# Kernel tuning notes

Measured on AMD Instinct MI355X. Metric: run time of the kernel, lower is better.

## Reference

```python
import jax, jax.numpy as jnp
import numpy as np
import math

B = 16384; IN_DIM = 512; OUT_DIM = 256
D_MODEL = 512; N_HEADS = 8; E_LAYERS = 3; D_FF = 2048
FACTOR = 5; EPS = 1e-5
E_HEAD = D_MODEL // N_HEADS


def setup_inputs() -> dict:
    key = jax.random.key(0)
    ks = jax.random.split(key, 16)
    def w(k, shape):
        return jax.random.normal(k, shape, dtype=jnp.float32) * 0.02
    return {
        "x": jax.random.normal(ks[0], (B, IN_DIM), dtype=jnp.float32),
        "w_in": w(ks[1], (IN_DIM, D_MODEL)), "b_in": jnp.zeros((D_MODEL,), jnp.float32),
        "wq": w(ks[2], (D_MODEL, D_MODEL)), "bq": jnp.zeros((D_MODEL,), jnp.float32),
        "wk": w(ks[3], (D_MODEL, D_MODEL)), "bk": jnp.zeros((D_MODEL,), jnp.float32),
        "wv": w(ks[4], (D_MODEL, D_MODEL)), "bv": jnp.zeros((D_MODEL,), jnp.float32),
        "wo": w(ks[5], (D_MODEL, D_MODEL)), "bo": jnp.zeros((D_MODEL,), jnp.float32),
        "conv1_w": w(ks[6], (E_LAYERS, D_MODEL, D_FF)), "conv1_b": jnp.zeros((E_LAYERS, D_FF), jnp.float32),
        "conv2_w": w(ks[7], (E_LAYERS, D_FF, D_MODEL)), "conv2_b": jnp.zeros((E_LAYERS, D_MODEL), jnp.float32),
        "n1_g": jnp.ones((E_LAYERS, D_MODEL), jnp.float32), "n1_b": jnp.zeros((E_LAYERS, D_MODEL), jnp.float32),
        "n2_g": jnp.ones((E_LAYERS, D_MODEL), jnp.float32), "n2_b": jnp.zeros((E_LAYERS, D_MODEL), jnp.float32),
        "norm_g": jnp.ones((D_MODEL,), jnp.float32), "norm_b": jnp.zeros((D_MODEL,), jnp.float32),
        "w1": w(ks[8], (D_MODEL, D_FF)), "b1": jnp.zeros((D_FF,), jnp.float32),
        "w2": w(ks[9], (D_FF, OUT_DIM)), "b2": jnp.zeros((OUT_DIM,), jnp.float32),
    }


def _layernorm(x, g, b):
    m = jnp.mean(x, axis=-1, keepdims=True)
    v = jnp.mean(jnp.square(x - m), axis=-1, keepdims=True)
    return (x - m) * jax.lax.rsqrt(v + EPS) * g + b


def _prob_attention(q, k, v):
    # q,k,v: [B,H,L,E]; Informer ProbAttention with mask_flag=False.
    Bq, H, L, Eh = q.shape
    L_K = k.shape[2]
    # static (Python-level) sparse-attention sizes, as in the source
    U_part = min(L_K, max(1, FACTOR * int(np.ceil(np.log(max(L_K, 1.1))))))
    u = min(L, max(1, FACTOR * int(np.ceil(np.log(max(L, 1.1))))))
    step = L_K // max(1, U_part)
    idx = jnp.arange(0, L_K, step)                      # deterministic key sample
    k_s = k[:, :, idx, :]                               # [B,H,S,E] (no L_Q expand needed)
    qk_s = jnp.einsum('bhle,bhse->bhls', q, k_s)        # sampled QK scores
    M = qk_s.max(-1) - qk_s.sum(-1) / L_K               # sparsity measure [B,H,L]
    _, top = jax.lax.top_k(M, u)                        # top-u query indices [B,H,u]
    q_r = jnp.take_along_axis(q, top[..., None], axis=2)  # gather Q_reduce [B,H,u,E]
    scale = 1.0 / math.sqrt(Eh)
    scores = jnp.einsum('bhue,bhke->bhuk', q_r, k) * scale
    attn = jax.nn.softmax(scores, axis=-1)
    upd = jnp.einsum('bhuk,bhkd->bhud', attn, v)        # [B,H,u,D]
    # initial context = mean of V (mask_flag=False), then scatter top-u rows
    ctx = jnp.broadcast_to(v.mean(axis=2, keepdims=True), (Bq, H, L, v.shape[-1]))
    bi = jnp.arange(Bq)[:, None, None]
    hi = jnp.arange(H)[None, :, None]
    return ctx.at[bi, hi, top].set(upd)


def _attention_layer(x, wq, bq, wk, bk, wv, bv, wo, bo):
    Bx, L, _ = x.shape
    def proj(w, b):
        return (x @ w + b).reshape(Bx, L, N_HEADS, E_HEAD).transpose(0, 2, 1, 3)
    ctx = _prob_attention(proj(wq, bq), proj(wk, bk), proj(wv, bv))
    ctx = ctx.transpose(0, 2, 1, 3).reshape(Bx, L, -1)
    return ctx @ wo + bo


def _forward(x, w_in, b_in, wq, bq, wk, bk, wv, bv, wo, bo,
             conv1_w, conv1_b, conv2_w, conv2_b,
             n1_g, n1_b, n2_g, n2_b, norm_g, norm_b, w1, b1, w2, b2):
    h = (x @ w_in + b_in)[:, None, :]  # [B, 1, d_model] -- seq_len hardwired to 1
    for i in range(E_LAYERS):
        # NOTE: attention projection weights are SHARED across layers (as in source)
        a = _attention_layer(h, wq, bq, wk, bk, wv, bv, wo, bo)
        h = _layernorm(h + a, n1_g[i], n1_b[i])
        y = jax.nn.gelu(h @ conv1_w[i] + conv1_b[i], approximate=False)  # 1x1 conv == linear
        y = y @ conv2_w[i] + conv2_b[i]
        h = _layernorm(h + y, n2_g[i], n2_b[i])
    h = _layernorm(h, norm_g, norm_b)[:, 0, :]
    o = jax.nn.gelu(h @ w1 + b1, approximate=False)
    return o @ w2 + b2


def reference(x, w_in, b_in, wq, bq, wk, bk, wv, bv, wo, bo,
              conv1_w, conv1_b, conv2_w, conv2_b,
              n1_g, n1_b, n2_g, n2_b, norm_g, norm_b, w1, b1, w2, b2):
    return _forward(x, w_in, b_in, wq, bq, wk, bk, wv, bv, wo, bo,
                    conv1_w, conv1_b, conv2_w, conv2_b,
                    n1_g, n1_b, n2_g, n2_b, norm_g, norm_b, w1, b1, w2, b2)
```

## Files before the change

### kernel.cpp

```cpp
#include <hip/hip_runtime.h>
#include <hip/hip_bf16.h>
#include <math.h>

#define B_ROWS 16384
#define DM 512
#define DFF 2048
#define DOUT 256
#define EPSV 1e-5f

typedef __hip_bfloat16 bf16;
typedef __attribute__((ext_vector_type(8))) short short8;
typedef __attribute__((ext_vector_type(4))) float f32x4;

__device__ __forceinline__ float gelu_f(float x) {
    return 0.5f * x * (1.0f + erff(x * 0.70710678118654752f));
}

__device__ __forceinline__ float bf2f(short s) {
    return __uint_as_float(((unsigned int)(unsigned short)s) << 16);
}

__device__ __forceinline__ void gload16(const void* g, void* l) {
    __builtin_amdgcn_global_load_lds((const __attribute__((address_space(1))) void*)g,
                                     (__attribute__((address_space(3))) void*)l, 16, 0, 0);
}

__device__ __forceinline__ int xcd_swz(int bid, int nwg) {
    const int cpx = nwg >> 3;
    return (bid & 7) * cpx + (bid >> 3);
}

template<bool GELU, bool OUTF, bool OUTB>
__global__ __launch_bounds__(256, 2)
void gemm_kernel(const bf16* __restrict__ A, const bf16* __restrict__ BT,
                 const float* __restrict__ bias,
                 float* __restrict__ Cf, bf16* __restrict__ Cb,
                 int M, int N, int K)
{
    __shared__ __align__(16) bf16 lA[2][128 * 32];
    __shared__ __align__(16) bf16 lB[2][128 * 32];

    const int t    = threadIdx.x;
    const int lane = t & 63;
    const int w    = t >> 6;
    const int wr   = w >> 1, wc = w & 1;
    const int fr   = lane & 15, kg = lane >> 4;

    int bid = xcd_swz(blockIdx.y * gridDim.x + blockIdx.x, gridDim.x * gridDim.y);
    const int bx = bid % gridDim.x, by = bid / gridDim.x;
    const long bm = (long)by * 128;
    const long bn = (long)bx * 128;

    const int lr = t >> 2;
    const int lc = (t & 3) * 8;

    const bf16* Ag0 = A + (bm + lr) * (long)K + lc;
    const bf16* Ag1 = Ag0 + 64L * K;
    const bf16* Bg0 = BT + (bn + lr) * (long)K + lc;
    const bf16* Bg1 = Bg0 + 64L * K;

    f32x4 acc[4][4];
#pragma unroll
    for (int i = 0; i < 4; i++)
#pragma unroll
        for (int j = 0; j < 4; j++) acc[i][j] = (f32x4){0.f, 0.f, 0.f, 0.f};

    const int nk = K >> 5;

    gload16(Ag0, &lA[0][t * 8]);
    gload16(Ag1, &lA[0][2048 + t * 8]);
    gload16(Bg0, &lB[0][t * 8]);
    gload16(Bg1, &lB[0][2048 + t * 8]);
    Ag0 += 32; Ag1 += 32; Bg0 += 32; Bg1 += 32;
    __syncthreads();

    int cur = 0;
    for (int kt = 0; kt < nk; ++kt) {
        if (kt + 1 < nk) {
            const int nxt = cur ^ 1;
            gload16(Ag0, &lA[nxt][t * 8]);
            gload16(Ag1, &lA[nxt][2048 + t * 8]);
            gload16(Bg0, &lB[nxt][t * 8]);
            gload16(Bg1, &lB[nxt][2048 + t * 8]);
            Ag0 += 32; Ag1 += 32; Bg0 += 32; Bg1 += 32;
        }

        short8 af[4], bv[4];
#pragma unroll
        for (int m = 0; m < 4; m++)
            af[m] = *(const short8*)(&lA[cur][(wr * 64 + m * 16 + fr) * 32 + kg * 8]);
#pragma unroll
        for (int n = 0; n < 4; n++)
            bv[n] = *(const short8*)(&lB[cur][(wc * 64 + n * 16 + fr) * 32 + kg * 8]);
#pragma unroll
        for (int m = 0; m < 4; m++)
#pragma unroll
            for (int n = 0; n < 4; n++)
                acc[m][n] = __builtin_amdgcn_mfma_f32_16x16x32_bf16(af[m], bv[n], acc[m][n], 0, 0, 0);

        __syncthreads();
        cur ^= 1;
    }

#pragma unroll
    for (int m = 0; m < 4; m++) {
        const long row0 = bm + wr * 64 + m * 16 + kg * 4;
#pragma unroll
        for (int n = 0; n < 4; n++) {
            const long col = bn + wc * 64 + n * 16 + fr;
            const float bias_v = bias ? bias[col] : 0.0f;
#pragma unroll
            for (int r = 0; r < 4; r++) {
                float v = acc[m][n][r] + bias_v;
                if (GELU) v = gelu_f(v);
                const long idx = (row0 + r) * (long)N + col;
                if (OUTF) Cf[idx] = v;
                if (OUTB) Cb[idx] = __float2bfloat16(v);
            }
        }
    }
}

template<bool HASADD, bool OUTF>
__global__ __launch_bounds__(256)
void ln_kernel(const float* __restrict__ x, const bf16* __restrict__ add,
               const float* __restrict__ g, const float* __restrict__ bb,
               float* __restrict__ outf, bf16* __restrict__ outb)
{
    const int w    = threadIdx.x >> 6;
    const int lane = threadIdx.x & 63;
    const long row = (long)blockIdx.x * 4 + w;
    const int c0   = lane * 8;

    const float* xr = x + row * DM + c0;
    float4 a0 = *(const float4*)xr;
    float4 a1 = *(const float4*)(xr + 4);
    float v[8] = {a0.x, a0.y, a0.z, a0.w, a1.x, a1.y, a1.z, a1.w};
    if (HASADD) {
        short8 ad = *(const short8*)(add + row * DM + c0);
#pragma unroll
        for (int j = 0; j < 8; j++) v[j] += bf2f(ad[j]);
    }
    float s = 0.f;
#pragma unroll
    for (int j = 0; j < 8; j++) s += v[j];
#pragma unroll
    for (int off = 32; off > 0; off >>= 1) s += __shfl_xor(s, off);
    const float mean = s * (1.0f / 512.0f);

    float q = 0.f;
#pragma unroll
    for (int j = 0; j < 8; j++) { v[j] -= mean; q += v[j] * v[j]; }
#pragma unroll
    for (int off = 32; off > 0; off >>= 1) q += __shfl_xor(q, off);
    const float rstd = rsqrtf(q * (1.0f / 512.0f) + EPSV);

    float4 g0 = *(const float4*)(g + c0);
    float4 g1 = *(const float4*)(g + c0 + 4);
    float4 b0 = *(const float4*)(bb + c0);
    float4 b1 = *(const float4*)(bb + c0 + 4);
    float y[8];
    y[0] = v[0] * rstd * g0.x + b0.x; y[1] = v[1] * rstd * g0.y + b0.y;
    y[2] = v[2] * rstd * g0.z + b0.z; y[3] = v[3] * rstd * g0.w + b0.w;
    y[4] = v[4] * rstd * g1.x + b1.x; y[5] = v[5] * rstd * g1.y + b1.y;
    y[6] = v[6] * rstd * g1.z + b1.z; y[7] = v[7] * rstd * g1.w + b1.w;

    if (OUTF) {
        float* orow = outf + row * DM + c0;
        *(float4*)orow       = make_float4(y[0], y[1], y[2], y[3]);
        *(float4*)(orow + 4) = make_float4(y[4], y[5], y[6], y[7]);
    }
    {
        bf16 tmpb[8];
#pragma unroll
        for (int j = 0; j < 8; j++) tmpb[j] = __float2bfloat16(y[j]);
        *(uint4*)(outb + row * DM + c0) = *(const uint4*)tmpb;
    }
}

__global__ __launch_bounds__(256)
void transpose_bf16_kernel(const float* __restrict__ src, bf16* __restrict__ dst, int K, int N)
{
    __shared__ float tile[32][33];
    const long boff = (long)blockIdx.z * K * N;
    src += boff; dst += boff;
    const int n0 = blockIdx.x * 32, k0 = blockIdx.y * 32;
    const int tx = threadIdx.x & 31, ty = threadIdx.x >> 5;
#pragma unroll
    for (int j = 0; j < 32; j += 8)
        tile[ty + j][tx] = src[(long)(k0 + ty + j) * N + n0 + tx];
    __syncthreads();
#pragma unroll
    for (int j = 0; j < 32; j += 8)
        dst[(long)(n0 + ty + j) * K + k0 + tx] = __float2bfloat16(tile[tx][ty + j]);
}

__global__ __launch_bounds__(256)
void cvt_kernel(const float* __restrict__ src, bf16* __restrict__ dst, long n4)
{
    const long i = (long)blockIdx.x * 256 + threadIdx.x;
    if (i >= n4) return;
    const float4 vv = *(const float4*)(src + i * 4);
    bf16 t[4] = {__float2bfloat16(vv.x), __float2bfloat16(vv.y),
                 __float2bfloat16(vv.z), __float2bfloat16(vv.w)};
    *(uint2*)(dst + i * 4) = *(const uint2*)t;
}

__global__ __launch_bounds__(256)
void ba_kernel(const float* __restrict__ bv, const float* __restrict__ wo,
               const float* __restrict__ bo, float* __restrict__ ba)
{
    const int n = blockIdx.x * 256 + threadIdx.x;
    float s = bo[n];
    for (int j = 0; j < DM; j++) s += bv[j] * wo[(long)j * DM + n];
    ba[n] = s;
}

extern "C" void kernel_launch(void* const* d_in, const int* in_sizes, int n_in,
                              void* d_out, int out_size, void* d_ws, size_t ws_size,
                              hipStream_t stream)
{
    const float* x       = (const float*)d_in[0];
    const float* w_in    = (const float*)d_in[1];
    const float* b_in    = (const float*)d_in[2];
    const float* wv      = (const float*)d_in[7];
    const float* bv      = (const float*)d_in[8];
    const float* wo      = (const float*)d_in[9];
    const float* bo      = (const float*)d_in[10];
    const float* conv1_w = (const float*)d_in[11];
    const float* conv1_b = (const float*)d_in[12];
    const float* conv2_w = (const float*)d_in[13];
    const float* conv2_b = (const float*)d_in[14];
    const float* n1_g    = (const float*)d_in[15];
    const float* n1_b    = (const float*)d_in[16];
    const float* n2_g    = (const float*)d_in[17];
    const float* n2_b    = (const float*)d_in[18];
    const float* norm_g  = (const float*)d_in[19];
    const float* norm_b  = (const float*)d_in[20];
    const float* w1      = (const float*)d_in[21];
    const float* b1      = (const float*)d_in[22];
    const float* w2      = (const float*)d_in[23];
    const float* b2      = (const float*)d_in[24];
    float* out = (float*)d_out;

    char* ws = (char*)d_ws;
    size_t off = 0;
    auto alloc = [&](size_t bytes) {
        char* p = ws + off;
        off += (bytes + 255) & ~(size_t)255;
        return p;
    };
    bf16*  xbf  = (bf16*) alloc((size_t)B_ROWS * DM * 2);
    float* h    = (float*)alloc((size_t)B_ROWS * DM * 4);
    bf16*  hbf  = (bf16*) alloc((size_t)B_ROWS * DM * 2);
    bf16*  tmpb = (bf16*) alloc((size_t)B_ROWS * DM * 2);
    bf16*  y1   = (bf16*) alloc((size_t)B_ROWS * DFF * 2);
    bf16*  winT = (bf16*) alloc((size_t)DM * DM * 2);
    bf16*  woT  = (bf16*) alloc((size_t)DM * DM * 2);
    bf16*  wvbf = (bf16*) alloc((size_t)DM * DM * 2);
    bf16*  WaT  = (bf16*) alloc((size_t)DM * DM * 2);
    float* ba   = (float*)alloc((size_t)DM * 4);
    bf16*  c1T  = (bf16*) alloc((size_t)3 * DFF * DM * 2);
    bf16*  c2T  = (bf16*) alloc((size_t)3 * DM * DFF * 2);
    bf16*  w1T  = (bf16*) alloc((size_t)DFF * DM * 2);
    bf16*  w2T  = (bf16*) alloc((size_t)DOUT * DFF * 2);

    dim3 blk(256);

    cvt_kernel<<<(B_ROWS * DM / 4 + 255) / 256, blk, 0, stream>>>(x, xbf, (long)B_ROWS * DM / 4);
    cvt_kernel<<<(DM * DM / 4 + 255) / 256, blk, 0, stream>>>(wv, wvbf, (long)DM * DM / 4);
    transpose_bf16_kernel<<<dim3(DM / 32, DM / 32, 1), blk, 0, stream>>>(w_in, winT, DM, DM);
    transpose_bf16_kernel<<<dim3(DM / 32, DM / 32, 1), blk, 0, stream>>>(wo, woT, DM, DM);
    transpose_bf16_kernel<<<dim3(DFF / 32, DM / 32, 3), blk, 0, stream>>>(conv1_w, c1T, DM, DFF);
    transpose_bf16_kernel<<<dim3(DM / 32, DFF / 32, 3), blk, 0, stream>>>(conv2_w, c2T, DFF, DM);
    transpose_bf16_kernel<<<dim3(DFF / 32, DM / 32, 1), blk, 0, stream>>>(w1, w1T, DM, DFF);
    transpose_bf16_kernel<<<dim3(DOUT / 32, DFF / 32, 1), blk, 0, stream>>>(w2, w2T, DFF, DOUT);
    ba_kernel<<<2, blk, 0, stream>>>(bv, wo, bo, ba);
    gemm_kernel<false, false, true><<<dim3(4, 4), blk, 0, stream>>>(
        woT, wvbf, nullptr, nullptr, WaT, DM, DM, DM);

    gemm_kernel<false, true, true><<<dim3(4, 128), blk, 0, stream>>>(
        xbf, winT, b_in, h, hbf, B_ROWS, DM, DM);

    for (int i = 0; i < 3; i++) {
        gemm_kernel<false, false, true><<<dim3(4, 128), blk, 0, stream>>>(
            hbf, WaT, ba, nullptr, tmpb, B_ROWS, DM, DM);
        ln_kernel<true, true><<<B_ROWS / 4, blk, 0, stream>>>(
            h, tmpb, n1_g + i * DM, n1_b + i * DM, h, hbf);
        gemm_kernel<true, false, true><<<dim3(16, 128), blk, 0, stream>>>(
            hbf, c1T + (size_t)i * DFF * DM, conv1_b + i * DFF, nullptr, y1, B_ROWS, DFF, DM);
        gemm_kernel<false, false, true><<<dim3(4, 128), blk, 0, stream>>>(
            y1, c2T + (size_t)i * DM * DFF, conv2_b + i * DM, nullptr, tmpb, B_ROWS, DM, DFF);
        ln_kernel<true, true><<<B_ROWS / 4, blk, 0, stream>>>(
            h, tmpb, n2_g + i * DM, n2_b + i * DM, h, hbf);
    }

    ln_kernel<false, false><<<B_ROWS / 4, blk, 0, stream>>>(
        h, nullptr, norm_g, norm_b, nullptr, hbf);
    gemm_kernel<true, false, true><<<dim3(16, 128), blk, 0, stream>>>(
        hbf, w1T, b1, nullptr, y1, B_ROWS, DFF, DM);
    gemm_kernel<false, true, false><<<dim3(2, 128), blk, 0, stream>>>(
        y1, w2T, b2, out, nullptr, B_ROWS, DOUT, DFF);
}
```

Baseline: 789.3 us.

## Add 256x256-tile 8-wave GEMM with GELU epilogue for FFN up-projections

Adds a new bf16 GEMM kernel with 256x256 block tiles, 512 threads, a 64-wide K step split into two halves, XOR-swizzled LDS, direct global-to-LDS loads and interleaved prefetch/MFMA phases separated by scheduling barriers. It replaces the 128x128 GEMM for the four d_model->d_ff GELU projections. The aim is more data reuse per block and better overlap of loads with MFMA work. The cost is 128 KB of LDS per block and a large accumulator register footprint, which may limit occupancy; the epilogue also writes scalar bf16 values without coalescing.

```diff
diff --git a/kernel.cpp b/kernel.cpp
--- a/kernel.cpp
+++ b/kernel.cpp
@@ -28,6 +28,134 @@
 __device__ __forceinline__ int xcd_swz(int bid, int nwg) {
     const int cpx = nwg >> 3;
     return (bid & 7) * cpx + (bid >> 3);
+}
+
+#define SBAR() do { __builtin_amdgcn_sched_barrier(0); \
+                    __builtin_amdgcn_s_barrier();      \
+                    __builtin_amdgcn_sched_barrier(0); } while (0)
+
+__global__ __launch_bounds__(512, 2)
+void gemm256_gelu_kernel(const bf16* __restrict__ A, const bf16* __restrict__ BT,
+                         const float* __restrict__ bias, bf16* __restrict__ Cb,
+                         int M, int N, int K)
+{
+    __shared__ __align__(16) bf16 lds[65536];
+    bf16* lA = lds;
+    bf16* lB = lds + 32768;
+
+    const int t    = threadIdx.x;
+    const int lane = t & 63;
+    const int w    = t >> 6;
+    const int wm   = w >> 2, wn = w & 3;
+    const int fr   = lane & 15, kg = lane >> 4;
+
+    const int bid = xcd_swz(blockIdx.y * gridDim.x + blockIdx.x, gridDim.x * gridDim.y);
+    const int bx = bid % gridDim.x, by = bid / gridDim.x;
+    const long bm = (long)by * 256;
+    const long bn = (long)bx * 256;
+
+    const int srow = t >> 2;
+    const int skc  = t & 3;
+
+#define STAGE_A(KT, KH) { const int b_ = (KT) & 1;                                         \
+    _Pragma("unroll") for (int j = 0; j < 2; ++j) {                                        \
+        const int lrow = j * 128 + srow;                                                   \
+        gload16(A + (bm + lrow) * (long)K + (KT) * 64 + (KH) * 32                          \
+                  + ((skc ^ ((lrow >> 1) & 3)) * 8),                                       \
+                lA + b_ * 16384 + (KH) * 8192 + lrow * 32 + skc * 8); } }
+#define STAGE_B(KT, KH) { const int b_ = (KT) & 1;                                         \
+    _Pragma("unroll") for (int j = 0; j < 2; ++j) {                                        \
+        const int lrow = j * 128 + srow;                                                   \
+        gload16(BT + (bn + lrow) * (long)K + (KT) * 64 + (KH) * 32                         \
+                  + ((skc ^ ((lrow >> 1) & 3)) * 8),                                       \
+                lB + b_ * 16384 + (KH) * 8192 + lrow * 32 + skc * 8); } }
+
+#define LDA(BUF, KS, AM) (*(const short8*)(lA + (BUF) * 16384 + (KS) * 8192               \
+        + (wm * 128 + (AM) * 16 + fr) * 32                                                 \
+        + ((kg ^ (((wm * 128 + (AM) * 16 + fr) >> 1) & 3)) * 8)))
+#define LDB(BUF, KS, AN) (*(const short8*)(lB + (BUF) * 16384 + (KS) * 8192               \
+        + (wn * 64 + (AN) * 16 + fr) * 32                                                  \
+        + ((kg ^ (((wn * 64 + (AN) * 16 + fr) >> 1) & 3)) * 8)))
+
+#define MFMA_PHASE(AMBASE)                                                                 \
+    __builtin_amdgcn_s_setprio(1);                                                         \
+    _Pragma("unroll") for (int i_ = 0; i_ < 4; ++i_) {                                     \
+        _Pragma("unroll") for (int an_ = 0; an_ < 4; ++an_)                                \
+            acc[(AMBASE) + i_][an_] = __builtin_amdgcn_mfma_f32_16x16x32_bf16(             \
+                afr[i_], bfr[an_], acc[(AMBASE) + i_][an_], 0, 0, 0); }                    \
+    __builtin_amdgcn_s_setprio(0);
+
+    f32x4 acc[8][4];
+#pragma unroll
+    for (int i = 0; i < 8; i++)
+#pragma unroll
+        for (int j = 0; j < 4; j++) acc[i][j] = (f32x4){0.f, 0.f, 0.f, 0.f};
+
+    const int NT = K >> 6;
+
+    STAGE_A(0, 0); STAGE_B(0, 0); STAGE_A(0, 1); STAGE_B(0, 1);
+    STAGE_A(1, 0); STAGE_B(1, 0);
+    asm volatile("s_waitcnt vmcnt(4)" ::: "memory");
+    SBAR();
+
+    for (int T = 0; T < NT; ++T) {
+        const int buf = T & 1;
+        short8 afr[4], bfr[4];
+
+#pragma unroll
+        for (int an = 0; an < 4; ++an) bfr[an] = LDB(buf, 0, an);
+#pragma unroll
+        for (int i = 0; i < 4; ++i) afr[i] = LDA(buf, 0, i);
+        if (T + 1 < NT) STAGE_A(T + 1, 1);
+        SBAR();
+        MFMA_PHASE(0);
+        SBAR();
+
+#pragma unroll
+        for (int i = 0; i < 4; ++i) afr[i] = LDA(buf, 0, 4 + i);
+        if (T + 1 < NT) STAGE_B(T + 1, 1);
+        SBAR();
+        MFMA_PHASE(4);
+        SBAR();
+
+#pragma unroll
+        for (int an = 0; an < 4; ++an) bfr[an] = LDB(buf, 1, an);
+#pragma unroll
+        for (int i = 0; i < 4; ++i) afr[i] = LDA(buf, 1, i);
+        if (T + 2 < NT) STAGE_A(T + 2, 0);
+        SBAR();
+        MFMA_PHASE(0);
+        SBAR();
+
+#pragma unroll
+        for (int i = 0; i < 4; ++i) afr[i] = LDA(buf, 1, 4 + i);
+        if (T + 2 < NT) STAGE_B(T + 2, 0);
+        SBAR();
+        MFMA_PHASE(4);
+        asm volatile("s_waitcnt vmcnt(4)" ::: "memory");
+        SBAR();
+    }
+    asm volatile("s_waitcnt vmcnt(0)" ::: "memory");
+
+#pragma unroll
+    for (int am = 0; am < 8; ++am) {
+        const long row0 = bm + wm * 128 + am * 16 + kg * 4;
+#pragma unroll
+        for (int an = 0; an < 4; ++an) {
+            const long col = bn + wn * 64 + an * 16 + fr;
+            const float bv_ = bias[col];
+#pragma unroll
+            for (int r = 0; r < 4; ++r) {
+                const float v = gelu_f(acc[am][an][r] + bv_);
+                Cb[(row0 + r) * (long)N + col] = __float2bfloat16(v);
+            }
+        }
+    }
+#undef STAGE_A
+#undef STAGE_B
+#undef LDA
+#undef LDB
+#undef MFMA_PHASE
 }
 
 template<bool GELU, bool OUTF, bool OUTB>
@@ -287,8 +415,8 @@
             hbf, WaT, ba, nullptr, tmpb, B_ROWS, DM, DM);
         ln_kernel<true, true><<<B_ROWS / 4, blk, 0, stream>>>(
             h, tmpb, n1_g + i * DM, n1_b + i * DM, h, hbf);
-        gemm_kernel<true, false, true><<<dim3(16, 128), blk, 0, stream>>>(
-            hbf, c1T + (size_t)i * DFF * DM, conv1_b + i * DFF, nullptr, y1, B_ROWS, DFF, DM);
+        gemm256_gelu_kernel<<<dim3(DFF / 256, B_ROWS / 256), dim3(512), 0, stream>>>(
+            hbf, c1T + (size_t)i * DFF * DM, conv1_b + i * DFF, y1, B_ROWS, DFF, DM);
         gemm_kernel<false, false, true><<<dim3(4, 128), blk, 0, stream>>>(
             y1, c2T + (size_t)i * DM * DFF, conv2_b + i * DM, nullptr, tmpb, B_ROWS, DM, DFF);
         ln_kernel<true, true><<<B_ROWS / 4, blk, 0, stream>>>(
@@ -297,8 +425,8 @@
 
     ln_kernel<false, false><<<B_ROWS / 4, blk, 0, stream>>>(
         h, nullptr, norm_g, norm_b, nullptr, hbf);
-    gemm_kernel<true, false, true><<<dim3(16, 128), blk, 0, stream>>>(
-        hbf, w1T, b1, nullptr, y1, B_ROWS, DFF, DM);
+    gemm256_gelu_kernel<<<dim3(DFF / 256, B_ROWS / 256), dim3(512), 0, stream>>>(
+        hbf, w1T, b1, y1, B_ROWS, DFF, DM);
     gemm_kernel<false, true, false><<<dim3(2, 128), blk, 0, stream>>>(
         y1, w2T, b2, out, nullptr, B_ROWS, DOUT, DFF);
 }
```

New measurement: 813.1 us. 3.0% more time.
